# Optimization experiments

Measured on AMD Instinct MI355X. Metric: run time of the kernel, lower is better.

Reference implementation:

```python
import jax, jax.numpy as jnp
import numpy as np

N = 100000
IN_C = 128
HID = 32   # 2*out_channels
OUT = 16
NEG_SLOPE = 0.2


def gat_layer(x, src, dst, n, W, a_src, a_dst, b):
    # x: [n, Cin] -> h: [n, Cout]
    h = x @ W
    alpha_s = h @ a_src  # [n]
    alpha_d = h @ a_dst  # [n]
    e = jax.nn.leaky_relu(alpha_s[src] + alpha_d[dst], NEG_SLOPE)  # [E]
    # softmax over edges grouped by destination node (self-loops ensure no empty groups)
    m = jax.ops.segment_max(e, dst, num_segments=n)
    ex = jnp.exp(e - m[dst])
    s = jax.ops.segment_sum(ex, dst, num_segments=n)
    alpha = ex / s[dst]  # [E]
    out = jax.ops.segment_sum(h[src] * alpha[:, None], dst, num_segments=n)
    return out + b


def setup_inputs() -> dict:
    key = jax.random.key(0)
    ks = jax.random.split(key, 16)
    x = jax.random.normal(ks[0], (N, IN_C), dtype=jnp.float32)
    edge_index = jax.random.randint(ks[1], (2, 1600000), 0, N, dtype=jnp.int64)

    def glorot(k, shape):
        fan = shape[0] + (shape[1] if len(shape) > 1 else 1)
        return jax.random.normal(k, shape, dtype=jnp.float32) * jnp.sqrt(2.0 / fan)

    return {
        "x": x,
        "edge_index": edge_index,
        "W1": glorot(ks[2], (IN_C, HID)),
        "a1_src": glorot(ks[3], (HID,)),
        "a1_dst": glorot(ks[4], (HID,)),
        "b1": jnp.zeros((HID,), dtype=jnp.float32),
        "W_mu": glorot(ks[5], (HID, OUT)),
        "a_mu_src": glorot(ks[6], (OUT,)),
        "a_mu_dst": glorot(ks[7], (OUT,)),
        "b_mu": jnp.zeros((OUT,), dtype=jnp.float32),
        "W_ls": glorot(ks[8], (HID, OUT)),
        "a_ls_src": glorot(ks[9], (OUT,)),
        "a_ls_dst": glorot(ks[10], (OUT,)),
        "b_ls": jnp.zeros((OUT,), dtype=jnp.float32),
    }


def reference(x, edge_index, W1, a1_src, a1_dst, b1,
              W_mu, a_mu_src, a_mu_dst, b_mu,
              W_ls, a_ls_src, a_ls_dst, b_ls):
    n = x.shape[0]
    # PyG GATConv default: add self-loops
    loop = jnp.arange(n, dtype=edge_index.dtype)
    src = jnp.concatenate([edge_index[0], loop])
    dst = jnp.concatenate([edge_index[1], loop])

    h = jax.nn.relu(gat_layer(x, src, dst, n, W1, a1_src, a1_dst, b1))
    mu = gat_layer(h, src, dst, n, W_mu, a_mu_src, a_mu_dst, b_mu)
    logstd = gat_layer(h, src, dst, n, W_ls, a_ls_src, a_ls_dst, b_ls)
    return (mu, logstd)
```

## Files before the change

### kernel.cpp

```cpp
#include <hip/hip_runtime.h>
#include <hip/hip_bf16.h>
#include <hip/hip_fp16.h>

typedef unsigned int u32;
typedef unsigned short u16;

__device__ __forceinline__ float lrelu(float v) {
    return v > 0.f ? v : 0.2f * v;
}

__device__ __forceinline__ float4 ldq_h16(const u16* __restrict__ row, int q) {
    uint2 u = ((const uint2*)row)[q];
    __half2 a = *(__half2*)&u.x;
    __half2 b = *(__half2*)&u.y;
    float2 fa = __half22float2(a);
    float2 fb = __half22float2(b);
    return make_float4(fa.x, fa.y, fb.x, fb.y);
}

__device__ __forceinline__ u32 pack2h(float x, float y) {
    __half2 h = __float22half2_rn(make_float2(x, y));
    return *(u32*)&h;
}

#define PCHUNK 4096
#define NW 256

__global__ __launch_bounds__(256) void g1p_kernel(
    const float* __restrict__ x, const float* __restrict__ W,
    const float* __restrict__ a_src, const float* __restrict__ a_dst,
    u16* __restrict__ h16, float* __restrict__ as_, float* __restrict__ ad_,
    const int* __restrict__ srcI, const int* __restrict__ dstI,
    u32* __restrict__ pairs, u32* __restrict__ bcur,
    int n, int E, int wsz, int cap, int pgrid)
{
    __shared__ float xs[64][132];
    __shared__ float Wl[128][32];
    __shared__ float asv[32], adv[32];
    __shared__ u32 lcount[NW];
    __shared__ u32 lbase[NW];
    int t = threadIdx.x;

    if ((int)blockIdx.x < pgrid) {
        int chunk = blockIdx.x * PCHUNK;
        lcount[t] = 0;
        __syncthreads();
        u32 pk[16]; int wv[16]; u32 rk[16]; bool val[16];
#pragma unroll
        for (int k = 0; k < 16; k++) {
            int i = chunk + k * 256 + t;
            val[k] = i < E;
            if (val[k]) {
                u32 s = (u32)srcI[i];
                u32 d = (u32)dstI[i];
                wv[k] = d / (u32)wsz;
                u32 dloc = d - (u32)wv[k] * (u32)wsz;
                pk[k] = (dloc << 17) | s;
                rk[k] = atomicAdd(&lcount[wv[k]], 1u);
            }
        }
        __syncthreads();
        if (lcount[t] > 0)
            lbase[t] = atomicAdd(&bcur[t], lcount[t]);
        __syncthreads();
#pragma unroll
        for (int k = 0; k < 16; k++) {
            if (val[k]) {
                u32 pos = lbase[wv[k]] + rk[k];
                if (pos < (u32)cap)
                    pairs[(size_t)wv[k] * cap + pos] = pk[k];
            }
        }
        return;
    }

    int rb = (blockIdx.x - pgrid) * 64;

    for (int i = t; i < 4096; i += 256) Wl[i >> 5][i & 31] = W[i];
    if (t < 32) { asv[t] = a_src[t]; adv[t] = a_dst[t]; }
    for (int i = t; i < 2048; i += 256) {
        int row = i >> 5, seg = i & 31;
        float4 v = make_float4(0.f, 0.f, 0.f, 0.f);
        if (rb + row < n)
            v = ((const float4*)(x + (size_t)(rb + row) * 128))[seg];
        int c = seg * 4;
        xs[row][c + 0] = v.x; xs[row][c + 1] = v.y;
        xs[row][c + 2] = v.z; xs[row][c + 3] = v.w;
    }
    __syncthreads();

    int tr = t >> 3;
    int tc = t & 7;
    float acc[2][4];
#pragma unroll
    for (int i = 0; i < 2; i++)
#pragma unroll
        for (int j = 0; j < 4; j++) acc[i][j] = 0.f;

#pragma unroll 4
    for (int k = 0; k < 128; k++) {
        float x0 = xs[tr][k];
        float x1 = xs[tr + 32][k];
        float4 wv = *(const float4*)&Wl[k][tc * 4];
        acc[0][0] += x0 * wv.x; acc[0][1] += x0 * wv.y;
        acc[0][2] += x0 * wv.z; acc[0][3] += x0 * wv.w;
        acc[1][0] += x1 * wv.x; acc[1][1] += x1 * wv.y;
        acc[1][2] += x1 * wv.z; acc[1][3] += x1 * wv.w;
    }

#pragma unroll
    for (int i = 0; i < 2; i++) {
        int r = rb + tr + i * 32;
        if (r < n) {
            uint2 p;
            p.x = pack2h(acc[i][0], acc[i][1]);
            p.y = pack2h(acc[i][2], acc[i][3]);
            *(uint2*)&h16[(size_t)r * 32 + tc * 4] = p;
        }
        float ps = 0.f, pd = 0.f;
#pragma unroll
        for (int j = 0; j < 4; j++) {
            int c = tc * 4 + j;
            ps += acc[i][j] * asv[c];
            pd += acc[i][j] * adv[c];
        }
        for (int m = 1; m < 8; m <<= 1) {
            ps += __shfl_xor(ps, m, 64);
            pd += __shfl_xor(pd, m, 64);
        }
        if (tc == 0 && r < n) { as_[r] = ps; ad_[r] = pd; }
    }
}

__global__ __launch_bounds__(256) void csr_window_kernel(
    const u32* __restrict__ pairs, const u32* __restrict__ bcur,
    u32* __restrict__ rowS, u32* __restrict__ deg, int* __restrict__ srcS,
    u32* __restrict__ perm,
    int n, int wsz, int cap)
{
    __shared__ u32 dw[512];
    __shared__ u32 cw[512];
    __shared__ u32 ts[256];
    __shared__ u32 hb[512];
    int grp = blockIdx.x;
    int t = threadIdx.x;
    int wlo = grp * wsz;
    int wnodes = n - wlo; if (wnodes < 0) wnodes = 0; if (wnodes > wsz) wnodes = wsz;
    u32 cnt = bcur[grp]; if (cnt > (u32)cap) cnt = (u32)cap;
    size_t base = (size_t)grp * cap;

    {
        int wlo_t = t * wsz;
        int wn_t = n - wlo_t; if (wn_t < 0) wn_t = 0; if (wn_t > wsz) wn_t = wsz;
        u32 c_t = bcur[t]; if (c_t > (u32)cap) c_t = (u32)cap;
        ts[t] = c_t + (u32)wn_t;
        __syncthreads();
        for (int o = 1; o < NW; o <<= 1) {
            u32 y = (t >= o) ? ts[t - o] : 0u;
            __syncthreads();
            ts[t] += y;
            __syncthreads();
        }
    }
    u32 wb = ts[grp] - (cnt + (u32)wnodes);
    __syncthreads();

    dw[t] = 0; dw[t + 256] = 0;
    hb[t] = 0; hb[t + 256] = 0;
    __syncthreads();
    for (u32 i = t; i < cnt; i += 256)
        atomicAdd(&dw[pairs[base + i] >> 17], 1u);
    __syncthreads();

    int i0 = 2 * t, i1 = 2 * t + 1;
    u32 e0 = (i0 < wnodes) ? dw[i0] + 1u : 0u;
    u32 e1 = (i1 < wnodes) ? dw[i1] + 1u : 0u;
    ts[t] = e0 + e1;
    __syncthreads();
    for (int o = 1; o < 256; o <<= 1) {
        u32 y = (t >= o) ? ts[t - o] : 0u;
        __syncthreads();
        ts[t] += y;
        __syncthreads();
    }
    u32 off = wb + ts[t] - (e0 + e1);
    if (i0 < wnodes) {
        u32 dgi = dw[i0];
        cw[i0] = off;
        rowS[wlo + i0] = off;
        deg[wlo + i0] = dgi;
        srcS[off + dgi] = wlo + i0;
    }
    u32 off1 = off + e0;
    if (i1 < wnodes) {
        u32 dgi = dw[i1];
        cw[i1] = off1;
        rowS[wlo + i1] = off1;
        deg[wlo + i1] = dgi;
        srcS[off1 + dgi] = wlo + i1;
    }
    __syncthreads();

    for (int i = t; i < wnodes; i += 256)
        atomicAdd(&hb[dw[i] < 511u ? dw[i] : 511u], 1u);
    __syncthreads();
    {
        u32 h0 = hb[2 * t], h1 = hb[2 * t + 1];
        ts[t] = h0 + h1;
        __syncthreads();
        for (int o = 1; o < 256; o <<= 1) {
            u32 y = (t >= o) ? ts[t - o] : 0u;
            __syncthreads();
            ts[t] += y;
            __syncthreads();
        }
        u32 b0 = ts[t] - (h0 + h1);
        hb[2 * t] = b0;
        hb[2 * t + 1] = b0 + h0;
    }
    __syncthreads();
    for (int i = t; i < wnodes; i += 256) {
        u32 dg = dw[i] < 511u ? dw[i] : 511u;
        u32 pos = atomicAdd(&hb[dg], 1u);
        perm[wlo + pos] = (u32)(wlo + i);
    }
    for (int i = wnodes + t; i < wsz; i += 256)
        perm[wlo + i] = 0x7fffffffu;
    __syncthreads();

    for (u32 i = t; i < cnt; i += 256) {
        u32 pr = pairs[base + i];
        u32 pos = atomicAdd(&cw[pr >> 17], 1u);
        srcS[pos] = (int)(pr & 0x1FFFFu);
    }
}

__global__ __launch_bounds__(256) void l1_fused_kernel(
    const u32* __restrict__ rowS, const u32* __restrict__ deg,
    const int* __restrict__ srcS, const u32* __restrict__ perm,
    const float* __restrict__ as_, const float* __restrict__ ad_,
    const u16* __restrict__ h16, const float* __restrict__ b1,
    float* __restrict__ h1r, int n, int ntot)
{
    int gid = blockIdx.x * 16 + (threadIdx.x >> 4);
    if (gid >= ntot) return;
    int d = (int)perm[gid];
    if (d >= n) return;
    int l  = threadIdx.x & 15;
    int e2 = l >> 3;
    int q  = l & 7;
    int gb = (threadIdx.x & 63) & 48;

    int beg = (int)rowS[d];
    int end = beg + (int)deg[d] + 1;
    float adv = ad_[d];

    float wsum = 0.f;
    float4 acc = make_float4(0.f, 0.f, 0.f, 0.f);

    for (int tb = beg; tb < end; tb += 16) {
        int j = tb + l;
        bool valid = j < end;
        int s = valid ? srcS[j] : 0;
        float p = valid ? __expf(fminf(lrelu(as_[s] + adv), 60.f)) : 0.f;
        int cnt = end - tb; if (cnt > 16) cnt = 16;
        for (int jj = 0; jj < cnt; jj += 2) {
            int idx = jj + e2;
            int sj  = __shfl(s, gb + idx, 64);
            float w = __shfl(p, gb + idx, 64);
            if (idx >= cnt) w = 0.f;
            wsum += w;
            float4 hv = ldq_h16(h16 + (size_t)sj * 32, q);
            acc.x += w * hv.x; acc.y += w * hv.y;
            acc.z += w * hv.z; acc.w += w * hv.w;
        }
    }
    wsum  += __shfl_xor(wsum, 8, 64);
    acc.x += __shfl_xor(acc.x, 8, 64);
    acc.y += __shfl_xor(acc.y, 8, 64);
    acc.z += __shfl_xor(acc.z, 8, 64);
    acc.w += __shfl_xor(acc.w, 8, 64);
    if (l < 8) {
        float inv = 1.f / wsum;
        float4 r;
        r.x = fmaxf(acc.x * inv + b1[4 * q + 0], 0.f);
        r.y = fmaxf(acc.y * inv + b1[4 * q + 1], 0.f);
        r.z = fmaxf(acc.z * inv + b1[4 * q + 2], 0.f);
        r.w = fmaxf(acc.w * inv + b1[4 * q + 3], 0.f);
        *(float4*)&h1r[(size_t)d * 32 + 4 * q] = r;
    }
}

__global__ __launch_bounds__(256) void gemm2_kernel(
    const float* __restrict__ h1r,
    const float* __restrict__ Wm, const float* __restrict__ Wl_,
    const float* __restrict__ ams, const float* __restrict__ amd,
    const float* __restrict__ alsb, const float* __restrict__ ald,
    u16* __restrict__ hmhl16, float2* __restrict__ attn2,
    float* __restrict__ amud, float* __restrict__ alsd, int n)
{
    __shared__ float hs[16][33];
    __shared__ float Wms[32][16], Wls[32][16];
    __shared__ float amsv[16], amdv[16], alsv[16], aldv[16];
    int t = threadIdx.x;
    int rb = blockIdx.x * 16;

    for (int i = t; i < 512; i += 256) {
        int k = i >> 4, c = i & 15;
        Wms[k][c] = Wm[i];
        Wls[k][c] = Wl_[i];
    }
    if (t < 16) {
        amsv[t] = ams[t]; amdv[t] = amd[t];
        alsv[t] = alsb[t]; aldv[t] = ald[t];
    }
    for (int i = t; i < 512; i += 256) {
        int r = i >> 5, k = i & 31;
        int gr = rb + r;
        hs[r][k] = (gr < n) ? h1r[(size_t)gr * 32 + k] : 0.f;
    }
    __syncthreads();

    int tr = t >> 4;
    int c = t & 15;
    float accm = 0.f, accl = 0.f;
#pragma unroll
    for (int k = 0; k < 32; k++) {
        float hv = hs[tr][k];
        accm += hv * Wms[k][c];
        accl += hv * Wls[k][c];
    }
    int r = rb + tr;
    if (r < n) {
        hmhl16[(size_t)r * 32 + c]      = __half_as_ushort(__float2half(accm));
        hmhl16[(size_t)r * 32 + 16 + c] = __half_as_ushort(__float2half(accl));
    }
    float pms = accm * amsv[c], pmd = accm * amdv[c];
    float pls = accl * alsv[c], pld = accl * aldv[c];
    for (int m = 1; m < 16; m <<= 1) {
        pms += __shfl_xor(pms, m, 64);
        pmd += __shfl_xor(pmd, m, 64);
        pls += __shfl_xor(pls, m, 64);
        pld += __shfl_xor(pld, m, 64);
    }
    if (c == 0 && r < n) {
        attn2[r] = make_float2(pms, pls);
        amud[r] = pmd;
        alsd[r] = pld;
    }
}

__global__ __launch_bounds__(256) void l2_fused_kernel(
    const u32* __restrict__ rowS, const u32* __restrict__ deg,
    const int* __restrict__ srcS, const u32* __restrict__ perm,
    const float2* __restrict__ attn2,
    const float* __restrict__ amud, const float* __restrict__ alsd,
    const u16* __restrict__ hmhl16,
    const float* __restrict__ bm, const float* __restrict__ bl,
    float* __restrict__ out, int n, int ntot)
{
    int gid = blockIdx.x * 16 + (threadIdx.x >> 4);
    if (gid >= ntot) return;
    int d = (int)perm[gid];
    if (d >= n) return;
    int l  = threadIdx.x & 15;
    int e2 = l >> 3;
    int q  = l & 7;
    int gb = (threadIdx.x & 63) & 48;
    bool isMu = q < 4;

    int beg = (int)rowS[d];
    int end = beg + (int)deg[d] + 1;
    float amdv = amud[d], aldv = alsd[d];

    float wsum = 0.f;
    float4 acc = make_float4(0.f, 0.f, 0.f, 0.f);

    for (int tb = beg; tb < end; tb += 16) {
        int j = tb + l;
        bool valid = j < end;
        int s = valid ? srcS[j] : 0;
        float2 a2 = valid ? attn2[s] : make_float2(0.f, 0.f);
        float pm = valid ? __expf(fminf(lrelu(a2.x + amdv), 60.f)) : 0.f;
        float pl = valid ? __expf(fminf(lrelu(a2.y + aldv), 60.f)) : 0.f;
        int cnt = end - tb; if (cnt > 16) cnt = 16;
        for (int jj = 0; jj < cnt; jj += 2) {
            int idx = jj + e2;
            int sj    = __shfl(s, gb + idx, 64);
            float pmj = __shfl(pm, gb + idx, 64);
            float plj = __shfl(pl, gb + idx, 64);
            float w = isMu ? pmj : plj;
            if (idx >= cnt) w = 0.f;
            wsum += w;
            float4 hv = ldq_h16(hmhl16 + (size_t)sj * 32, q);
            acc.x += w * hv.x; acc.y += w * hv.y;
            acc.z += w * hv.z; acc.w += w * hv.w;
        }
    }
    wsum  += __shfl_xor(wsum, 8, 64);
    acc.x += __shfl_xor(acc.x, 8, 64);
    acc.y += __shfl_xor(acc.y, 8, 64);
    acc.z += __shfl_xor(acc.z, 8, 64);
    acc.w += __shfl_xor(acc.w, 8, 64);
    if (l < 8) {
        float inv = 1.f / wsum;
        if (q < 4) {
            float4 r;
            r.x = acc.x * inv + bm[4 * q + 0];
            r.y = acc.y * inv + bm[4 * q + 1];
            r.z = acc.z * inv + bm[4 * q + 2];
            r.w = acc.w * inv + bm[4 * q + 3];
            *(float4*)&out[(size_t)d * 16 + 4 * q] = r;
        } else {
            int qc = 4 * (q - 4);
            float4 r;
            r.x = acc.x * inv + bl[qc + 0];
            r.y = acc.y * inv + bl[qc + 1];
            r.z = acc.z * inv + bl[qc + 2];
            r.w = acc.w * inv + bl[qc + 3];
            *(float4*)&out[(size_t)n * 16 + (size_t)d * 16 + qc] = r;
        }
    }
}

extern "C" void kernel_launch(void* const* d_in, const int* in_sizes, int n_in,
                              void* d_out, int out_size, void* d_ws, size_t ws_size,
                              hipStream_t stream)
{
    const float* x   = (const float*)d_in[0];
    const int*   ei  = (const int*)d_in[1];
    const float* W1  = (const float*)d_in[2];
    const float* a1s = (const float*)d_in[3];
    const float* a1d = (const float*)d_in[4];
    const float* b1  = (const float*)d_in[5];
    const float* Wm  = (const float*)d_in[6];
    const float* ams = (const float*)d_in[7];
    const float* amd = (const float*)d_in[8];
    const float* bm  = (const float*)d_in[9];
    const float* Wl  = (const float*)d_in[10];
    const float* als = (const float*)d_in[11];
    const float* ald = (const float*)d_in[12];
    const float* bl  = (const float*)d_in[13];

    int n  = in_sizes[0] / 128;
    int E  = in_sizes[1] / 2;
    int Et = E + n;
    int wsz = (n + NW - 1) / NW;
    int cap = E / NW + 3072;
    int ntot = NW * wsz;
    const int* srcI = ei;
    const int* dstI = ei + E;

    float* ws = (float*)d_ws;
    u16*    h16   = (u16*)ws;
    u16*    hmhl16 = (u16*)(ws + (size_t)16 * n);
    float*  h1r  = ws + (size_t)32 * n;
    u32*    pairs = (u32*)(ws + (size_t)32 * n);
    float*  as_  = ws + (size_t)64 * n;
    float*  ad_  = ws + (size_t)65 * n;
    float2* attn2 = (float2*)(ws + (size_t)64 * n);
    float*  amud = ws + (size_t)66 * n;
    float*  alsd = ws + (size_t)67 * n;
    u32*    deg  = (u32*)(ws + (size_t)68 * n);
    u32*    bcur = (u32*)(ws + (size_t)69 * n);
    u32*    rowS = (u32*)(ws + (size_t)70 * n);
    int*    srcS = (int*)(ws + (size_t)71 * n);
    u32*    perm = (u32*)(ws + (size_t)71 * n + Et);

    int pgrid = (E + PCHUNK - 1) / PCHUNK;
    int gblocks = (n + 63) / 64;

    hipMemsetAsync(bcur, 0, NW * sizeof(u32), stream);

    g1p_kernel<<<pgrid + gblocks, 256, 0, stream>>>(
        x, W1, a1s, a1d, h16, as_, ad_,
        srcI, dstI, pairs, bcur, n, E, wsz, cap, pgrid);

    csr_window_kernel<<<NW, 256, 0, stream>>>(pairs, bcur,
                                              rowS, deg, srcS, perm,
                                              n, wsz, cap);

    l1_fused_kernel<<<(ntot + 15) / 16, 256, 0, stream>>>(rowS, deg, srcS, perm,
                                                          as_, ad_, h16, b1,
                                                          h1r, n, ntot);

    gemm2_kernel<<<(n + 15) / 16, 256, 0, stream>>>(h1r, Wm, Wl, ams, amd, als, ald,
                                                    hmhl16, attn2, amud, alsd, n);

    l2_fused_kernel<<<(ntot + 15) / 16, 256, 0, stream>>>(rowS, deg, srcS, perm,
                                                          attn2, amud, alsd,
                                                          hmhl16, bm, bl,
                                                          (float*)d_out, n, ntot);
}
```

Measured before the change: 254.7 us.

## Fuse layer-1 aggregation with layer-2 GEMM and attention projections

Merges the layer-1 attention aggregation kernel with the second-layer GEMM kernel. The aggregated, ReLU'd hidden rows stay in shared memory and are multiplied by the mu/logstd weights in the same block. This removes the h1r global round trip and one kernel launch. The as_/ad_ buffers move to a separate workspace region so the fused kernel's attn2 writes do not overwrite attention logits other blocks are still reading. The cost is per-block weight loading into shared memory, a block-wide barrier after the irregular gather loop, and scattered writes by permuted node index.

```diff
diff --git a/kernel.cpp b/kernel.cpp
--- a/kernel.cpp
+++ b/kernel.cpp
@@ -235,25 +235,48 @@
     }
 }
 
-__global__ __launch_bounds__(256) void l1_fused_kernel(
+__global__ __launch_bounds__(256) void l1g2_kernel(
     const u32* __restrict__ rowS, const u32* __restrict__ deg,
     const int* __restrict__ srcS, const u32* __restrict__ perm,
     const float* __restrict__ as_, const float* __restrict__ ad_,
     const u16* __restrict__ h16, const float* __restrict__ b1,
-    float* __restrict__ h1r, int n, int ntot)
+    const float* __restrict__ Wm, const float* __restrict__ Wl_,
+    const float* __restrict__ ams, const float* __restrict__ amd,
+    const float* __restrict__ alsb, const float* __restrict__ ald,
+    u16* __restrict__ hmhl16, float2* __restrict__ attn2,
+    float* __restrict__ amud, float* __restrict__ alsd,
+    int n, int ntot)
 {
-    int gid = blockIdx.x * 16 + (threadIdx.x >> 4);
-    if (gid >= ntot) return;
-    int d = (int)perm[gid];
-    if (d >= n) return;
-    int l  = threadIdx.x & 15;
+    __shared__ float hs[16][36];
+    __shared__ float Wms[32][16], Wls[32][16];
+    __shared__ float amsv[16], amdv[16], alsv[16], aldv[16];
+    __shared__ int dsl[16];
+    int t = threadIdx.x;
+
+    for (int i = t; i < 512; i += 256) {
+        Wms[i >> 4][i & 15] = Wm[i];
+        Wls[i >> 4][i & 15] = Wl_[i];
+    }
+    if (t < 16) {
+        amsv[t] = ams[t]; amdv[t] = amd[t];
+        alsv[t] = alsb[t]; aldv[t] = ald[t];
+    }
+
+    int gid = blockIdx.x * 16 + (t >> 4);
+    int d = (gid < ntot) ? (int)perm[gid] : 0x7fffffff;
+    bool live = (u32)d < (u32)n;
+    int l  = t & 15;
     int e2 = l >> 3;
     int q  = l & 7;
-    int gb = (threadIdx.x & 63) & 48;
-
-    int beg = (int)rowS[d];
-    int end = beg + (int)deg[d] + 1;
-    float adv = ad_[d];
+    int gb = (t & 63) & 48;
+
+    int beg = 0, end = 0;
+    float adv = 0.f;
+    if (live) {
+        beg = (int)rowS[d];
+        end = beg + (int)deg[d] + 1;
+        adv = ad_[d];
+    }
 
     float wsum = 0.f;
     float4 acc = make_float4(0.f, 0.f, 0.f, 0.f);
@@ -280,49 +303,22 @@
     acc.y += __shfl_xor(acc.y, 8, 64);
     acc.z += __shfl_xor(acc.z, 8, 64);
     acc.w += __shfl_xor(acc.w, 8, 64);
-    if (l < 8) {
+
+    if (l == 0) dsl[t >> 4] = live ? d : -1;
+    if (live && l < 8) {
         float inv = 1.f / wsum;
         float4 r;
         r.x = fmaxf(acc.x * inv + b1[4 * q + 0], 0.f);
         r.y = fmaxf(acc.y * inv + b1[4 * q + 1], 0.f);
         r.z = fmaxf(acc.z * inv + b1[4 * q + 2], 0.f);
         r.w = fmaxf(acc.w * inv + b1[4 * q + 3], 0.f);
-        *(float4*)&h1r[(size_t)d * 32 + 4 * q] = r;
-    }
-}
-
-__global__ __launch_bounds__(256) void gemm2_kernel(
-    const float* __restrict__ h1r,
-    const float* __restrict__ Wm, const float* __restrict__ Wl_,
-    const float* __restrict__ ams, const float* __restrict__ amd,
-    const float* __restrict__ alsb, const float* __restrict__ ald,
-    u16* __restrict__ hmhl16, float2* __restrict__ attn2,
-    float* __restrict__ amud, float* __restrict__ alsd, int n)
-{
-    __shared__ float hs[16][33];
-    __shared__ float Wms[32][16], Wls[32][16];
-    __shared__ float amsv[16], amdv[16], alsv[16], aldv[16];
-    int t = threadIdx.x;
-    int rb = blockIdx.x * 16;
-
-    for (int i = t; i < 512; i += 256) {
-        int k = i >> 4, c = i & 15;
-        Wms[k][c] = Wm[i];
-        Wls[k][c] = Wl_[i];
-    }
-    if (t < 16) {
-        amsv[t] = ams[t]; amdv[t] = amd[t];
-        alsv[t] = alsb[t]; aldv[t] = ald[t];
-    }
-    for (int i = t; i < 512; i += 256) {
-        int r = i >> 5, k = i & 31;
-        int gr = rb + r;
-        hs[r][k] = (gr < n) ? h1r[(size_t)gr * 32 + k] : 0.f;
+        *(float4*)&hs[t >> 4][4 * q] = r;
     }
     __syncthreads();
 
     int tr = t >> 4;
-    int c = t & 15;
+    int c  = t & 15;
+    int r2 = dsl[tr];
     float accm = 0.f, accl = 0.f;
 #pragma unroll
     for (int k = 0; k < 32; k++) {
@@ -330,10 +326,9 @@
         accm += hv * Wms[k][c];
         accl += hv * Wls[k][c];
     }
-    int r = rb + tr;
-    if (r < n) {
-        hmhl16[(size_t)r * 32 + c]      = __half_as_ushort(__float2half(accm));
-        hmhl16[(size_t)r * 32 + 16 + c] = __half_as_ushort(__float2half(accl));
+    if (r2 >= 0) {
+        hmhl16[(size_t)r2 * 32 + c]      = __half_as_ushort(__float2half(accm));
+        hmhl16[(size_t)r2 * 32 + 16 + c] = __half_as_ushort(__float2half(accl));
     }
     float pms = accm * amsv[c], pmd = accm * amdv[c];
     float pls = accl * alsv[c], pld = accl * aldv[c];
@@ -343,10 +338,10 @@
         pls += __shfl_xor(pls, m, 64);
         pld += __shfl_xor(pld, m, 64);
     }
-    if (c == 0 && r < n) {
-        attn2[r] = make_float2(pms, pls);
-        amud[r] = pmd;
-        alsd[r] = pld;
+    if (c == 0 && r2 >= 0) {
+        attn2[r2] = make_float2(pms, pls);
+        amud[r2] = pmd;
+        alsd[r2] = pld;
     }
 }
 
@@ -454,10 +449,7 @@
     float* ws = (float*)d_ws;
     u16*    h16   = (u16*)ws;
     u16*    hmhl16 = (u16*)(ws + (size_t)16 * n);
-    float*  h1r  = ws + (size_t)32 * n;
     u32*    pairs = (u32*)(ws + (size_t)32 * n);
-    float*  as_  = ws + (size_t)64 * n;
-    float*  ad_  = ws + (size_t)65 * n;
     float2* attn2 = (float2*)(ws + (size_t)64 * n);
     float*  amud = ws + (size_t)66 * n;
     float*  alsd = ws + (size_t)67 * n;
@@ -466,6 +458,8 @@
     u32*    rowS = (u32*)(ws + (size_t)70 * n);
     int*    srcS = (int*)(ws + (size_t)71 * n);
     u32*    perm = (u32*)(ws + (size_t)71 * n + Et);
+    float*  as_  = ws + (size_t)71 * n + Et + ntot;
+    float*  ad_  = as_ + n;
 
     int pgrid = (E + PCHUNK - 1) / PCHUNK;
     int gblocks = (n + 63) / 64;
@@ -480,12 +474,10 @@
                                               rowS, deg, srcS, perm,
                                               n, wsz, cap);
 
-    l1_fused_kernel<<<(ntot + 15) / 16, 256, 0, stream>>>(rowS, deg, srcS, perm,
-                                                          as_, ad_, h16, b1,
-                                                          h1r, n, ntot);
-
-    gemm2_kernel<<<(n + 15) / 16, 256, 0, stream>>>(h1r, Wm, Wl, ams, amd, als, ald,
-                                                    hmhl16, attn2, amud, alsd, n);
+    l1g2_kernel<<<(ntot + 15) / 16, 256, 0, stream>>>(
+        rowS, deg, srcS, perm, as_, ad_, h16, b1,
+        Wm, Wl, ams, amd, als, ald,
+        hmhl16, attn2, amud, alsd, n, ntot);
 
     l2_fused_kernel<<<(ntot + 15) / 16, 256, 0, stream>>>(rowS, deg, srcS, perm,
                                                           attn2, amud, alsd,
```

Result: faster. 246.8 us (-3.1%).
